# Kernel tuning notes

Hardware: AMD Instinct MI355X
Metric: run time of the kernel (lower is better)

Reference implementation:

```python
import jax, jax.numpy as jnp
import numpy as np

N = 50000      # nodes
E = 800000     # edges (before self-loops)
F_IN = 128     # num_features
HID = 32       # hidden channels per head (conv1)
HEADS = 4      # conv1 heads
C = 40         # classes (conv2 out channels)
OUT_HEADS = 1  # conv2 heads
NEG_SLOPE = 0.2


def setup_inputs() -> dict:
    key = jax.random.key(0)
    ks = jax.random.split(key, 10)
    x = jax.random.normal(ks[0], (N, F_IN), jnp.float32)
    edge_index = jax.random.randint(ks[1], (2, E), 0, N, jnp.int32)
    s1 = 1.0 / np.sqrt(F_IN).astype(np.float32)
    s1h = 1.0 / np.sqrt(HID).astype(np.float32)
    s2 = 1.0 / np.sqrt(HEADS * HID).astype(np.float32)
    s2c = 1.0 / np.sqrt(C).astype(np.float32)
    W1 = jax.random.normal(ks[2], (F_IN, HEADS * HID), jnp.float32) * s1
    att_src1 = jax.random.normal(ks[3], (HEADS, HID), jnp.float32) * s1h
    att_dst1 = jax.random.normal(ks[4], (HEADS, HID), jnp.float32) * s1h
    bias1 = jnp.zeros((HEADS * HID,), jnp.float32)
    W2 = jax.random.normal(ks[5], (HEADS * HID, OUT_HEADS * C), jnp.float32) * s2
    att_src2 = jax.random.normal(ks[6], (OUT_HEADS, C), jnp.float32) * s2c
    att_dst2 = jax.random.normal(ks[7], (OUT_HEADS, C), jnp.float32) * s2c
    bias2 = jnp.zeros((C,), jnp.float32)
    return {"x": x, "edge_index": edge_index,
            "W1": W1, "att_src1": att_src1, "att_dst1": att_dst1, "bias1": bias1,
            "W2": W2, "att_src2": att_src2, "att_dst2": att_dst2, "bias2": bias2}


def gat_layer(h_in, src, dst, W, a_src, a_dst, bias, heads, out_ch, concat):
    """PyG GATConv (v1) in inference mode (no dropout on attention)."""
    n = h_in.shape[0]
    h = (h_in @ W).reshape(n, heads, out_ch)              # [N,H,F]
    e_src = jnp.einsum('nhf,hf->nh', h, a_src)            # [N,H]
    e_dst = jnp.einsum('nhf,hf->nh', h, a_dst)            # [N,H]
    alpha = jax.nn.leaky_relu(e_src[src] + e_dst[dst], NEG_SLOPE)  # [E,H]
    # segment softmax over destination-node neighborhoods
    amax = jax.ops.segment_max(alpha, dst, num_segments=n)
    amax = jnp.where(jnp.isfinite(amax), amax, 0.0)
    ex = jnp.exp(alpha - amax[dst])
    denom = jax.ops.segment_sum(ex, dst, num_segments=n)
    coef = ex / (denom[dst] + 1e-16)                      # [E,H]
    # scatter-aggregate weighted source messages
    out = jax.ops.segment_sum(h[src] * coef[:, :, None], dst, num_segments=n)  # [N,H,F]
    out = out.reshape(n, heads * out_ch) if concat else out.mean(axis=1)
    return out + bias


def reference(x, edge_index, W1, att_src1, att_dst1, bias1, W2, att_src2, att_dst2, bias2):
    n = x.shape[0]
    loop = jnp.arange(n, dtype=edge_index.dtype)          # GATConv adds self-loops
    src = jnp.concatenate([edge_index[0], loop])
    dst = jnp.concatenate([edge_index[1], loop])
    h = jax.nn.elu(gat_layer(x, src, dst, W1, att_src1, att_dst1, bias1, HEADS, HID, True))
    out = gat_layer(h, src, dst, W2, att_src2, att_dst2, bias2, OUT_HEADS, C, False)
    return (jax.nn.log_softmax(out, axis=1), jax.nn.softmax(out, axis=1))
```

## Files before the change

kernel.cpp:

```cpp
#include <hip/hip_runtime.h>
#include <hip/hip_bf16.h>

#define F1   128
#define H1   4
#define C2   40
#define NEG  0.2f
#define BN   16
#define DS   96

typedef __hip_bfloat16 bf16;
typedef float f32x2 __attribute__((ext_vector_type(2)));

__device__ __forceinline__ float ldf(const void* p, size_t i, int isbf) {
    return isbf ? __bfloat162float(((const bf16*)p)[i]) : ((const float*)p)[i];
}
__device__ __forceinline__ float lrelu(float a) { return a > 0.f ? a : NEG * a; }

__device__ __forceinline__ void up2(unsigned g, float& lo, float& hi) {
    lo = __uint_as_float(g << 16);
    hi = __uint_as_float(g & 0xffff0000u);
}
__device__ __forceinline__ f32x2 up2v(unsigned g) {
    f32x2 r;
    r.x = __uint_as_float(g << 16);
    r.y = __uint_as_float(g & 0xffff0000u);
    return r;
}

__global__ void k_prep(const unsigned short* __restrict__ x, int* __restrict__ deg,
                       int N, int* __restrict__ flag) {
    int i = blockIdx.x * 256 + threadIdx.x;
    if (i < N) deg[i] = 0;
    if (blockIdx.x == 0) {
        __shared__ int sh[256];
        int cnt = 0;
        for (int k = threadIdx.x; k < 8192; k += 256)
            if (((x[k] >> 7) & 0xFF) >= 160) cnt++;
        sh[threadIdx.x] = cnt;
        __syncthreads();
        for (int s = 128; s > 0; s >>= 1) {
            if (threadIdx.x < s) sh[threadIdx.x] += sh[threadIdx.x + s];
            __syncthreads();
        }
        if (threadIdx.x == 0) flag[0] = (sh[0] < 100) ? 1 : 0;
    }
}

__global__ void k_gemm1(const void* __restrict__ x, const void* __restrict__ W1,
                        const void* __restrict__ as1, const void* __restrict__ ad1,
                        const int* __restrict__ flag, const int* __restrict__ ei,
                        int E, int ET, int* __restrict__ deg, int* __restrict__ ebuf2,
                        bf16* __restrict__ h1b, float* __restrict__ es1,
                        float* __restrict__ ed1, int N) {
    int per = (ET + gridDim.x - 1) / gridDim.x;
    int he0 = blockIdx.x * per;
    int he1 = he0 + per; if (he1 > ET) he1 = ET;
    for (int e = he0 + threadIdx.x; e < he1; e += 256) {
        int s, d;
        if (e < E) { s = ei[e]; d = ei[E + e]; }
        else       { s = e - E; d = e - E; }
        int pos = atomicAdd(&deg[d], 1);
        if (pos < DS) ebuf2[d * DS + pos] = s;
    }
    __shared__ float xs[BN][F1];
    const int isbf = flag[0];
    int n0 = blockIdx.x * BN, t = threadIdx.x;
    for (int i = t; i < BN * F1; i += 256) {
        int nn = i >> 7, kk = i & 127;
        int n = n0 + nn; if (n >= N) n = N - 1;
        xs[nn][kk] = ldf(x, (size_t)n * F1 + kk, isbf);
    }
    __syncthreads();
    int col = t & 127, nh = t >> 7;
    float a[8] = {0.f, 0.f, 0.f, 0.f, 0.f, 0.f, 0.f, 0.f};
    if (isbf) {
        const bf16* W = (const bf16*)W1;
#pragma unroll 2
        for (int k = 0; k < F1; k += 4) {
            float w0 = __bfloat162float(W[(size_t)k * F1 + col]);
            float w1 = __bfloat162float(W[(size_t)(k + 1) * F1 + col]);
            float w2 = __bfloat162float(W[(size_t)(k + 2) * F1 + col]);
            float w3 = __bfloat162float(W[(size_t)(k + 3) * F1 + col]);
#pragma unroll
            for (int j = 0; j < 8; j++) {
                float4 xv = *(const float4*)&xs[nh + 2 * j][k];
                a[j] = fmaf(xv.x, w0, a[j]);
                a[j] = fmaf(xv.y, w1, a[j]);
                a[j] = fmaf(xv.z, w2, a[j]);
                a[j] = fmaf(xv.w, w3, a[j]);
            }
        }
    } else {
        const float* W = (const float*)W1;
#pragma unroll 2
        for (int k = 0; k < F1; k += 4) {
            float w0 = W[(size_t)k * F1 + col];
            float w1 = W[(size_t)(k + 1) * F1 + col];
            float w2 = W[(size_t)(k + 2) * F1 + col];
            float w3 = W[(size_t)(k + 3) * F1 + col];
#pragma unroll
            for (int j = 0; j < 8; j++) {
                float4 xv = *(const float4*)&xs[nh + 2 * j][k];
                a[j] = fmaf(xv.x, w0, a[j]);
                a[j] = fmaf(xv.y, w1, a[j]);
                a[j] = fmaf(xv.z, w2, a[j]);
                a[j] = fmaf(xv.w, w3, a[j]);
            }
        }
    }
    float asv = ldf(as1, col, isbf), adv = ldf(ad1, col, isbf);
    int h = col >> 5;
#pragma unroll
    for (int j = 0; j < 8; j++) {
        int n = n0 + nh + 2 * j;
        float s = a[j] * asv, dd = a[j] * adv;
#pragma unroll
        for (int off = 16; off > 0; off >>= 1) {
            s += __shfl_down(s, off, 32);
            dd += __shfl_down(dd, off, 32);
        }
        if (n < N) {
            h1b[(size_t)n * F1 + col] = __float2bfloat16(a[j]);
            if ((t & 31) == 0) { es1[n * H1 + h] = s; ed1[n * H1 + h] = dd; }
        }
    }
}

__global__ void __launch_bounds__(256) k_l1(
        const int* __restrict__ deg, const int* __restrict__ ebuf2,
        const float* __restrict__ es1, const float* __restrict__ ed1,
        const uint4* __restrict__ h1p4, const void* __restrict__ b1,
        const void* __restrict__ W2, const void* __restrict__ as2,
        const void* __restrict__ ad2, const int* __restrict__ flag,
        bf16* __restrict__ h2b, float* __restrict__ es2, float* __restrict__ ed2,
        int N) {
    int w = threadIdx.x >> 6, l = threadIdx.x & 63;
    int d = blockIdx.x * 4 + w; if (d >= N) d = N - 1;
    int cnt = deg[d]; if (cnt > DS) cnt = DS;
    int start = d * DS;

    __shared__ int   s_sh[4][DS];
    __shared__ float ev_sh[4][4][DS + 4];
    __shared__ float hs[4][144];

    float4 edv = *(const float4*)&ed1[(size_t)d * 4];
    float t0 = 0.f, t1 = 0.f, t2 = 0.f, t3 = 0.f;
    if (l < cnt) {
        int s = ebuf2[start + l];
        s_sh[w][l] = s;
        float4 es4 = *(const float4*)&es1[(size_t)s * 4];
        float v0 = __expf(lrelu(es4.x + edv.x));
        float v1 = __expf(lrelu(es4.y + edv.y));
        float v2 = __expf(lrelu(es4.z + edv.z));
        float v3 = __expf(lrelu(es4.w + edv.w));
        ev_sh[w][0][l] = v0; ev_sh[w][1][l] = v1;
        ev_sh[w][2][l] = v2; ev_sh[w][3][l] = v3;
        t0 = v0; t1 = v1; t2 = v2; t3 = v3;
    }
    if (cnt > 64) {
        int l2 = 64 + l;
        if (l2 < cnt) {
            int s = ebuf2[start + l2];
            s_sh[w][l2] = s;
            float4 es4 = *(const float4*)&es1[(size_t)s * 4];
            float v0 = __expf(lrelu(es4.x + edv.x));
            float v1 = __expf(lrelu(es4.y + edv.y));
            float v2 = __expf(lrelu(es4.z + edv.z));
            float v3 = __expf(lrelu(es4.w + edv.w));
            ev_sh[w][0][l2] = v0; ev_sh[w][1][l2] = v1;
            ev_sh[w][2][l2] = v2; ev_sh[w][3][l2] = v3;
            t0 += v0; t1 += v1; t2 += v2; t3 += v3;
        }
    }
#pragma unroll
    for (int off = 32; off > 0; off >>= 1) {
        t0 += __shfl_xor(t0, off, 64);
        t1 += __shfl_xor(t1, off, 64);
        t2 += __shfl_xor(t2, off, 64);
        t3 += __shfl_xor(t3, off, 64);
    }
    __syncthreads();

    int q = l >> 4, c16 = l & 15, h = c16 >> 2;
    f32x2 acc[4] = {{0.f, 0.f}, {0.f, 0.f}, {0.f, 0.f}, {0.f, 0.f}};
    for (int i = 0; i < cnt; i += 16) {
#pragma unroll
        for (int u = 0; u < 4; u++) {
            int e = i + q + 4 * u;
            int ec = min(e, cnt - 1);
            float evh = (e < cnt) ? ev_sh[w][h][ec] : 0.f;
            int s = s_sh[w][ec];
            uint4 g = h1p4[(size_t)s * 16 + c16];
            f32x2 ev2 = {evh, evh};
            acc[0] += ev2 * up2v(g.x);
            acc[1] += ev2 * up2v(g.y);
            acc[2] += ev2 * up2v(g.z);
            acc[3] += ev2 * up2v(g.w);
        }
    }

#pragma unroll
    for (int off = 16; off <= 32; off <<= 1) {
#pragma unroll
        for (int jj = 0; jj < 4; jj++) {
            acc[jj].x += __shfl_xor(acc[jj].x, off, 64);
            acc[jj].y += __shfl_xor(acc[jj].y, off, 64);
        }
    }

    const int isbf = flag[0];
    float dsum = (h == 0) ? t0 : (h == 1) ? t1 : (h == 2) ? t2 : t3;
    if (q == 0) {
        float inv = 1.f / (dsum + 1e-16f);
#pragma unroll
        for (int j = 0; j < 8; j++) {
            int col = c16 * 8 + j;
            float av = (j & 1) ? acc[j >> 1].y : acc[j >> 1].x;
            float v = av * inv + ldf(b1, col, isbf);
            hs[w][col + (col >> 3)] = v > 0.f ? v : (__expf(v) - 1.f);
        }
    }
    __syncthreads();
    float a2 = 0.f;
    if (l < C2) {
        if (isbf) {
            const bf16* W = (const bf16*)W2;
#pragma unroll 8
            for (int k = 0; k < F1; k++)
                a2 = fmaf(hs[w][k + (k >> 3)], __bfloat162float(W[(size_t)k * C2 + l]), a2);
        } else {
            const float* W = (const float*)W2;
#pragma unroll 8
            for (int k = 0; k < F1; k++)
                a2 = fmaf(hs[w][k + (k >> 3)], W[(size_t)k * C2 + l], a2);
        }
        h2b[(size_t)d * C2 + l] = __float2bfloat16(a2);
    }
    float ps = (l < C2) ? a2 * ldf(as2, l, isbf) : 0.f;
    float pd = (l < C2) ? a2 * ldf(ad2, l, isbf) : 0.f;
#pragma unroll
    for (int off = 32; off > 0; off >>= 1) {
        ps += __shfl_xor(ps, off, 64);
        pd += __shfl_xor(pd, off, 64);
    }
    if (l == 0) { es2[d] = ps; ed2[d] = pd; }
}

__global__ void __launch_bounds__(256) k_l2(
        const int* __restrict__ deg, const int* __restrict__ ebuf2,
        const float* __restrict__ es2, const float* __restrict__ ed2,
        const unsigned* __restrict__ h2p, const void* __restrict__ b2,
        const int* __restrict__ flag, void* __restrict__ out, int N) {
    int w = threadIdx.x >> 6, l = threadIdx.x & 63;
    int d = blockIdx.x * 4 + w; if (d >= N) d = N - 1;
    int cnt = deg[d]; if (cnt > DS) cnt = DS;
    int start = d * DS;
    float edd = ed2[d];

    __shared__ int   s_sh2[4][DS];
    __shared__ float x_sh[4][DS];

    float xv = 0.f;
    if (l < cnt) {
        int s = ebuf2[start + l];
        s_sh2[w][l] = s;
        xv = __expf(lrelu(es2[s] + edd));
        x_sh[w][l] = xv;
    }
    float dsum = xv;
    if (cnt > 64) {
        int l2 = 64 + l;
        if (l2 < cnt) {
            int s = ebuf2[start + l2];
            s_sh2[w][l2] = s;
            float x2 = __expf(lrelu(es2[s] + edd));
            x_sh[w][l2] = x2;
            dsum += x2;
        }
    }
#pragma unroll
    for (int off = 32; off > 0; off >>= 1) dsum += __shfl_xor(dsum, off, 64);
    __syncthreads();

    int half = l >> 5, j = l & 31;
    float acc0 = 0.f, acc1 = 0.f;
    if (j < 20) {
        for (int i = 0; i < cnt; i += 16) {
#pragma unroll
            for (int u = 0; u < 8; u++) {
                int e = i + half * 8 + u;
                int ec = min(e, cnt - 1);
                float x = (e < cnt) ? x_sh[w][ec] : 0.f;
                int s = s_sh2[w][ec];
                unsigned g = h2p[(size_t)s * 20 + j];
                float lo, hi; up2(g, lo, hi);
                acc0 = fmaf(x, lo, acc0);
                acc1 = fmaf(x, hi, acc1);
            }
        }
        acc0 += __shfl_xor(acc0, 32, 64);
        acc1 += __shfl_xor(acc1, 32, 64);
    }

    const int isbf = flag[0];
    float inv = 1.f / (dsum + 1e-16f);
    float v0 = -1e30f, v1 = -1e30f;
    if (l < 20) {
        v0 = acc0 * inv + ldf(b2, 2 * l, isbf);
        v1 = acc1 * inv + ldf(b2, 2 * l + 1, isbf);
    }
    float m = fmaxf(v0, v1);
#pragma unroll
    for (int off = 16; off > 0; off >>= 1) m = fmaxf(m, __shfl_xor(m, off, 32));
    float sv = (l < 20) ? __expf(v0 - m) + __expf(v1 - m) : 0.f;
#pragma unroll
    for (int off = 16; off > 0; off >>= 1) sv += __shfl_xor(sv, off, 32);
    float lse = m + __logf(sv);
    if (l < 20) {
        float ls0 = v0 - lse, ls1 = v1 - lse;
        size_t base = (size_t)d * C2 + 2 * l, halfo = (size_t)N * C2;
        if (isbf) {
            bf16* o = (bf16*)out;
            o[base] = __float2bfloat16(ls0);
            o[base + 1] = __float2bfloat16(ls1);
            o[halfo + base] = __float2bfloat16(__expf(ls0));
            o[halfo + base + 1] = __float2bfloat16(__expf(ls1));
        } else {
            float* o = (float*)out;
            o[base] = ls0;
            o[base + 1] = ls1;
            o[halfo + base] = __expf(ls0);
            o[halfo + base + 1] = __expf(ls1);
        }
    }
}

extern "C" void kernel_launch(void* const* d_in, const int* in_sizes, int n_in,
                              void* d_out, int out_size, void* d_ws, size_t ws_size,
                              hipStream_t stream) {
    const int N  = in_sizes[0] / F1;
    const int E  = in_sizes[1] / 2;
    const int ET = E + N;
    const int NB = (N + 255) / 256;

    const void* x   = d_in[0];
    const int*  ei  = (const int*)d_in[1];
    const void* W1  = d_in[2];
    const void* as1 = d_in[3];
    const void* ad1 = d_in[4];
    const void* b1  = d_in[5];
    const void* W2  = d_in[6];
    const void* as2 = d_in[7];
    const void* ad2 = d_in[8];
    const void* b2  = d_in[9];

    float* ws = (float*)d_ws;
    auto al4 = [](size_t v) { return (v + 3) & ~(size_t)3; };
    size_t o = 0;
    bf16*  h1b  = (bf16*)(ws + o); o = al4(o + (size_t)64 * N);
    float* es1  = ws + o; o = al4(o + (size_t)H1 * N);
    float* ed1  = ws + o; o = al4(o + (size_t)H1 * N);
    bf16*  h2b  = (bf16*)(ws + o); o = al4(o + (size_t)20 * N);
    float* es2  = ws + o; o = al4(o + N);
    float* ed2  = ws + o; o = al4(o + N);
    int*   deg  = (int*)(ws + o); o = al4(o + N);
    int*   flag = (int*)(ws + o); o = al4(o + 4);
    int*   ebuf2 = (int*)(ws + o); o = al4(o + (size_t)DS * N);

    k_prep<<<NB, 256, 0, stream>>>((const unsigned short*)x, deg, N, flag);
    k_gemm1<<<(N + BN - 1) / BN, 256, 0, stream>>>(x, W1, as1, ad1, flag, ei, E, ET,
                                                   deg, ebuf2, h1b, es1, ed1, N);
    k_l1<<<(N + 3) / 4, 256, 0, stream>>>(deg, ebuf2, es1, ed1, (const uint4*)h1b,
                                          b1, W2, as2, ad2, flag, h2b, es2, ed2, N);
    k_l2<<<(N + 3) / 4, 256, 0, stream>>>(deg, ebuf2, es2, ed2, (const unsigned*)h2b,
                                          b2, flag, d_out, N);
}
```

Measured before the change: 286.0 us.

## Compute layer-1 projection with bf16 MFMA using split-bf16 for fp32 inputs

Replaces the scalar FMA GEMM for x@W1 with 16x16x32 bf16 MFMA instructions. A new small kernel transposes W1 and splits it into high and low bf16 parts, so fp32 inputs get near-fp32 accuracy from three MFMAs per tile. Blocks now cover 32 nodes instead of 16, which halves the grid and changes how the fused edge-bucketing loop is split. Separately, the layer-2 projection in k_l1 drops its padded shared layout and reads hs as float4. The cost is one extra launch and extra MFMA work on the fp32 path.

```diff
diff --git a/kernel.cpp b/kernel.cpp
--- a/kernel.cpp
+++ b/kernel.cpp
@@ -5,16 +5,25 @@
 #define H1   4
 #define C2   40
 #define NEG  0.2f
-#define BN   16
 #define DS   96
 
 typedef __hip_bfloat16 bf16;
 typedef float f32x2 __attribute__((ext_vector_type(2)));
+typedef short s16x8 __attribute__((ext_vector_type(8)));
+typedef float f32x4 __attribute__((ext_vector_type(4)));
 
 __device__ __forceinline__ float ldf(const void* p, size_t i, int isbf) {
     return isbf ? __bfloat162float(((const bf16*)p)[i]) : ((const float*)p)[i];
 }
 __device__ __forceinline__ float lrelu(float a) { return a > 0.f ? a : NEG * a; }
+
+__device__ __forceinline__ unsigned short f2bfb(float f, float& back) {
+    unsigned u = __float_as_uint(f);
+    unsigned r = u + 0x7FFFu + ((u >> 16) & 1u);
+    unsigned short h = (unsigned short)(r >> 16);
+    back = __uint_as_float((unsigned)h << 16);
+    return h;
+}
 
 __device__ __forceinline__ void up2(unsigned g, float& lo, float& hi) {
     lo = __uint_as_float(g << 16);
@@ -46,12 +55,29 @@
     }
 }
 
-__global__ void k_gemm1(const void* __restrict__ x, const void* __restrict__ W1,
-                        const void* __restrict__ as1, const void* __restrict__ ad1,
-                        const int* __restrict__ flag, const int* __restrict__ ei,
-                        int E, int ET, int* __restrict__ deg, int* __restrict__ ebuf2,
-                        bf16* __restrict__ h1b, float* __restrict__ es1,
-                        float* __restrict__ ed1, int N) {
+__global__ void k_wprep(const void* __restrict__ W1, const int* __restrict__ flag,
+                        unsigned short* __restrict__ w1t_hi,
+                        unsigned short* __restrict__ w1t_lo) {
+    int idx = blockIdx.x * 256 + threadIdx.x;
+    int k = idx >> 7, c = idx & 127;
+    const int isbf = flag[0];
+    float v = ldf(W1, idx, isbf);
+    float back;
+    unsigned short hi = f2bfb(v, back);
+    float d2;
+    unsigned short lo = f2bfb(v - back, d2);
+    w1t_hi[c * 128 + k] = hi;
+    w1t_lo[c * 128 + k] = isbf ? (unsigned short)0 : lo;
+}
+
+__global__ void __launch_bounds__(256) k_gemm1(
+        const void* __restrict__ x, const unsigned short* __restrict__ w1t_hi,
+        const unsigned short* __restrict__ w1t_lo,
+        const void* __restrict__ as1, const void* __restrict__ ad1,
+        const int* __restrict__ flag, const int* __restrict__ ei,
+        int E, int ET, int* __restrict__ deg, int* __restrict__ ebuf2,
+        bf16* __restrict__ h1b, float* __restrict__ es1, float* __restrict__ ed1,
+        int N) {
     int per = (ET + gridDim.x - 1) / gridDim.x;
     int he0 = blockIdx.x * per;
     int he1 = he0 + per; if (he1 > ET) he1 = ET;
@@ -62,66 +88,92 @@
         int pos = atomicAdd(&deg[d], 1);
         if (pos < DS) ebuf2[d * DS + pos] = s;
     }
-    __shared__ float xs[BN][F1];
     const int isbf = flag[0];
-    int n0 = blockIdx.x * BN, t = threadIdx.x;
-    for (int i = t; i < BN * F1; i += 256) {
-        int nn = i >> 7, kk = i & 127;
-        int n = n0 + nn; if (n >= N) n = N - 1;
-        xs[nn][kk] = ldf(x, (size_t)n * F1 + kk, isbf);
-    }
-    __syncthreads();
-    int col = t & 127, nh = t >> 7;
-    float a[8] = {0.f, 0.f, 0.f, 0.f, 0.f, 0.f, 0.f, 0.f};
-    if (isbf) {
-        const bf16* W = (const bf16*)W1;
-#pragma unroll 2
-        for (int k = 0; k < F1; k += 4) {
-            float w0 = __bfloat162float(W[(size_t)k * F1 + col]);
-            float w1 = __bfloat162float(W[(size_t)(k + 1) * F1 + col]);
-            float w2 = __bfloat162float(W[(size_t)(k + 2) * F1 + col]);
-            float w3 = __bfloat162float(W[(size_t)(k + 3) * F1 + col]);
+    int t = threadIdx.x, wv = t >> 6, l = t & 63;
+    int r0 = (wv & 1) * 16, c0 = (wv >> 1) * 64;
+    int lr = l & 15, q = l >> 4;
+    int n0 = blockIdx.x * 32;
+    int rowa = n0 + r0 + lr; if (rowa >= N) rowa = N - 1;
+
+    const bf16*  xb = (const bf16*)x;
+    const float* xf = (const float*)x;
+    f32x4 acc[4] = {};
+
+#pragma unroll
+    for (int ks = 0; ks < 4; ks++) {
+        int kb = ks * 32 + q * 8;
+        s16x8 ahi, alo;
+        if (isbf) {
+            ahi = *(const s16x8*)&xb[(size_t)rowa * 128 + kb];
+        } else {
+            const float* xr = xf + (size_t)rowa * 128 + kb;
+            float4 v0 = *(const float4*)xr;
+            float4 v1 = *(const float4*)(xr + 4);
+            float vv[8] = {v0.x, v0.y, v0.z, v0.w, v1.x, v1.y, v1.z, v1.w};
 #pragma unroll
             for (int j = 0; j < 8; j++) {
-                float4 xv = *(const float4*)&xs[nh + 2 * j][k];
-                a[j] = fmaf(xv.x, w0, a[j]);
-                a[j] = fmaf(xv.y, w1, a[j]);
-                a[j] = fmaf(xv.z, w2, a[j]);
-                a[j] = fmaf(xv.w, w3, a[j]);
-            }
-        }
-    } else {
-        const float* W = (const float*)W1;
-#pragma unroll 2
-        for (int k = 0; k < F1; k += 4) {
-            float w0 = W[(size_t)k * F1 + col];
-            float w1 = W[(size_t)(k + 1) * F1 + col];
-            float w2 = W[(size_t)(k + 2) * F1 + col];
-            float w3 = W[(size_t)(k + 3) * F1 + col];
-#pragma unroll
-            for (int j = 0; j < 8; j++) {
-                float4 xv = *(const float4*)&xs[nh + 2 * j][k];
-                a[j] = fmaf(xv.x, w0, a[j]);
-                a[j] = fmaf(xv.y, w1, a[j]);
-                a[j] = fmaf(xv.z, w2, a[j]);
-                a[j] = fmaf(xv.w, w3, a[j]);
-            }
-        }
-    }
-    float asv = ldf(as1, col, isbf), adv = ldf(ad1, col, isbf);
-    int h = col >> 5;
-#pragma unroll
-    for (int j = 0; j < 8; j++) {
-        int n = n0 + nh + 2 * j;
-        float s = a[j] * asv, dd = a[j] * adv;
-#pragma unroll
-        for (int off = 16; off > 0; off >>= 1) {
-            s += __shfl_down(s, off, 32);
-            dd += __shfl_down(dd, off, 32);
-        }
-        if (n < N) {
-            h1b[(size_t)n * F1 + col] = __float2bfloat16(a[j]);
-            if ((t & 31) == 0) { es1[n * H1 + h] = s; ed1[n * H1 + h] = dd; }
+                float back;
+                unsigned short hb = f2bfb(vv[j], back);
+                float d2;
+                unsigned short lb = f2bfb(vv[j] - back, d2);
+                ahi[j] = (short)hb;
+                alo[j] = (short)lb;
+            }
+        }
+#pragma unroll
+        for (int f = 0; f < 4; f++) {
+            int col = c0 + f * 16 + lr;
+            s16x8 bh = *(const s16x8*)&w1t_hi[(size_t)col * 128 + kb];
+            acc[f] = __builtin_amdgcn_mfma_f32_16x16x32_bf16(ahi, bh, acc[f], 0, 0, 0);
+            if (!isbf) {
+                s16x8 bl = *(const s16x8*)&w1t_lo[(size_t)col * 128 + kb];
+                acc[f] = __builtin_amdgcn_mfma_f32_16x16x32_bf16(alo, bh, acc[f], 0, 0, 0);
+                acc[f] = __builtin_amdgcn_mfma_f32_16x16x32_bf16(ahi, bl, acc[f], 0, 0, 0);
+            }
+        }
+    }
+
+    float asv[4], adv[4];
+#pragma unroll
+    for (int f = 0; f < 4; f++) {
+        asv[f] = ldf(as1, c0 + f * 16 + lr, isbf);
+        adv[f] = ldf(ad1, c0 + f * 16 + lr, isbf);
+    }
+    float ps0[4], ps1[4], pd0[4], pd1[4];
+#pragma unroll
+    for (int r = 0; r < 4; r++) {
+        int rw = n0 + r0 + q * 4 + r;
+        ps0[r] = acc[0][r] * asv[0] + acc[1][r] * asv[1];
+        ps1[r] = acc[2][r] * asv[2] + acc[3][r] * asv[3];
+        pd0[r] = acc[0][r] * adv[0] + acc[1][r] * adv[1];
+        pd1[r] = acc[2][r] * adv[2] + acc[3][r] * adv[3];
+        if (rw < N) {
+#pragma unroll
+            for (int f = 0; f < 4; f++)
+                h1b[(size_t)rw * 128 + c0 + f * 16 + lr] = __float2bfloat16(acc[f][r]);
+        }
+    }
+#pragma unroll
+    for (int off = 1; off < 16; off <<= 1) {
+#pragma unroll
+        for (int r = 0; r < 4; r++) {
+            ps0[r] += __shfl_xor(ps0[r], off, 64);
+            ps1[r] += __shfl_xor(ps1[r], off, 64);
+            pd0[r] += __shfl_xor(pd0[r], off, 64);
+            pd1[r] += __shfl_xor(pd1[r], off, 64);
+        }
+    }
+    if (lr == 0) {
+        int h0 = c0 >> 5;
+#pragma unroll
+        for (int r = 0; r < 4; r++) {
+            int rw = n0 + r0 + q * 4 + r;
+            if (rw < N) {
+                es1[rw * H1 + h0]     = ps0[r];
+                es1[rw * H1 + h0 + 1] = ps1[r];
+                ed1[rw * H1 + h0]     = pd0[r];
+                ed1[rw * H1 + h0 + 1] = pd1[r];
+            }
         }
     }
 }
@@ -141,7 +193,7 @@
 
     __shared__ int   s_sh[4][DS];
     __shared__ float ev_sh[4][4][DS + 4];
-    __shared__ float hs[4][144];
+    __shared__ float hs[4][F1];
 
     float4 edv = *(const float4*)&ed1[(size_t)d * 4];
     float t0 = 0.f, t1 = 0.f, t2 = 0.f, t3 = 0.f;
@@ -217,7 +269,7 @@
             int col = c16 * 8 + j;
             float av = (j & 1) ? acc[j >> 1].y : acc[j >> 1].x;
             float v = av * inv + ldf(b1, col, isbf);
-            hs[w][col + (col >> 3)] = v > 0.f ? v : (__expf(v) - 1.f);
+            hs[w][col] = v > 0.f ? v : (__expf(v) - 1.f);
         }
     }
     __syncthreads();
@@ -225,14 +277,26 @@
     if (l < C2) {
         if (isbf) {
             const bf16* W = (const bf16*)W2;
-#pragma unroll 8
-            for (int k = 0; k < F1; k++)
-                a2 = fmaf(hs[w][k + (k >> 3)], __bfloat162float(W[(size_t)k * C2 + l]), a2);
+#pragma unroll
+            for (int k4 = 0; k4 < 32; k4++) {
+                float4 hv = *(const float4*)&hs[w][k4 * 4];
+                int kb = k4 * 4;
+                a2 = fmaf(hv.x, __bfloat162float(W[(size_t)kb * C2 + l]), a2);
+                a2 = fmaf(hv.y, __bfloat162float(W[(size_t)(kb + 1) * C2 + l]), a2);
+                a2 = fmaf(hv.z, __bfloat162float(W[(size_t)(kb + 2) * C2 + l]), a2);
+                a2 = fmaf(hv.w, __bfloat162float(W[(size_t)(kb + 3) * C2 + l]), a2);
+            }
         } else {
             const float* W = (const float*)W2;
-#pragma unroll 8
-            for (int k = 0; k < F1; k++)
-                a2 = fmaf(hs[w][k + (k >> 3)], W[(size_t)k * C2 + l], a2);
+#pragma unroll
+            for (int k4 = 0; k4 < 32; k4++) {
+                float4 hv = *(const float4*)&hs[w][k4 * 4];
+                int kb = k4 * 4;
+                a2 = fmaf(hv.x, W[(size_t)kb * C2 + l], a2);
+                a2 = fmaf(hv.y, W[(size_t)(kb + 1) * C2 + l], a2);
+                a2 = fmaf(hv.z, W[(size_t)(kb + 2) * C2 + l], a2);
+                a2 = fmaf(hv.w, W[(size_t)(kb + 3) * C2 + l], a2);
+            }
         }
         h2b[(size_t)d * C2 + l] = __float2bfloat16(a2);
     }
@@ -366,10 +430,13 @@
     int*   deg  = (int*)(ws + o); o = al4(o + N);
     int*   flag = (int*)(ws + o); o = al4(o + 4);
     int*   ebuf2 = (int*)(ws + o); o = al4(o + (size_t)DS * N);
+    unsigned short* w1t_hi = (unsigned short*)(ws + o); o = al4(o + 8192);
+    unsigned short* w1t_lo = (unsigned short*)(ws + o); o = al4(o + 8192);
 
     k_prep<<<NB, 256, 0, stream>>>((const unsigned short*)x, deg, N, flag);
-    k_gemm1<<<(N + BN - 1) / BN, 256, 0, stream>>>(x, W1, as1, ad1, flag, ei, E, ET,
-                                                   deg, ebuf2, h1b, es1, ed1, N);
+    k_wprep<<<64, 256, 0, stream>>>(W1, flag, w1t_hi, w1t_lo);
+    k_gemm1<<<(N + 31) / 32, 256, 0, stream>>>(x, w1t_hi, w1t_lo, as1, ad1, flag,
+                                               ei, E, ET, deg, ebuf2, h1b, es1, ed1, N);
     k_l1<<<(N + 3) / 4, 256, 0, stream>>>(deg, ebuf2, es1, ed1, (const uint4*)h1b,
                                           b1, W2, as2, ad2, flag, h2b, es2, ed2, N);
     k_l2<<<(N + 3) / 4, 256, 0, stream>>>(deg, ebuf2, es2, ed2, (const unsigned*)h2b,
```

New measurement: 324.8 us. 1.14x slower.
